# Kernel optimization log

Hardware: AMD Instinct MI355X
Metric: run time of the kernel (lower is better)

Reference implementation:

```python
import jax, jax.numpy as jnp
import numpy as np

DROPOUT_P = 0.0  # undefined global `dropout_p` in source; pinned to 0 (identity) for determinism


def setup_inputs() -> dict:
    key = jax.random.key(0)
    k1, k2, k3 = jax.random.split(key, 3)
    B, Lq, Lk, D = 16, 4096, 4096, 64
    return {
        "query": jax.random.normal(k1, (B, Lq, D), dtype=jnp.float32),
        "key": jax.random.normal(k2, (B, Lk, D), dtype=jnp.float32),
        "value": jax.random.normal(k3, (B, Lk, D), dtype=jnp.float32),
        "scale_factor": jnp.ones((1,), dtype=jnp.float32),
    }


def reference(query, key, value, scale_factor):
    # scores: [B, Lq, Lk] -- the large HBM-materialized intermediate
    scores = jnp.einsum("bqd,bkd->bqk", query, key) / scale_factor
    probs = jax.nn.softmax(scores, axis=-1)
    # dropout with p = DROPOUT_P = 0.0 is the identity
    out = jnp.einsum("bqk,bkd->bqd", probs, value)
    return out
```

## Files before the change

### kernel.cpp

```cpp
#include <hip/hip_runtime.h>
#include <hip/hip_fp16.h>

typedef _Float16 half2_t __attribute__((ext_vector_type(2)));
typedef _Float16 half4_t __attribute__((ext_vector_type(4)));
typedef _Float16 half8_t __attribute__((ext_vector_type(8)));
typedef float   float4_t __attribute__((ext_vector_type(4)));

static __device__ __forceinline__ half2_t cvt_pk(float a, float b) {
    return __builtin_bit_cast(half2_t, __builtin_amdgcn_cvt_pkrtz(a, b));
}
static __device__ __forceinline__ half4_t cvt_pk4(float a, float b, float c, float d) {
    half2_t lo = cvt_pk(a, b), hi = cvt_pk(c, d);
    half4_t r;
    r[0] = lo[0]; r[1] = lo[1]; r[2] = hi[0]; r[3] = hi[1];
    return r;
}
static __device__ __forceinline__ half8_t cvt_pk8(const float4& a, const float4& b) {
    half4_t lo = cvt_pk4(a.x, a.y, a.z, a.w);
    half4_t hi = cvt_pk4(b.x, b.y, b.z, b.w);
    return __builtin_shufflevector(lo, hi, 0, 1, 2, 3, 4, 5, 6, 7);
}

namespace {
constexpr int kB       = 16;
constexpr int kL       = 4096;
constexpr int kD       = 64;
constexpr int kQTile   = 128;
constexpr int kBK      = 64;
constexpr int kTiles   = kL / kBK;
constexpr int kTileH   = kBK * kD;
constexpr int kKStride = 72;
constexpr int kVStride = 68;
constexpr size_t kWsHalves = (size_t)kB * kTiles * kTileH;
}


__global__ __launch_bounds__(256) void prep_kv(const float* __restrict__ K,
                                               const float* __restrict__ V,
                                               _Float16* __restrict__ Kws,
                                               _Float16* __restrict__ Vws)
{
    int blk = blockIdx.x;
    const int tid = threadIdx.x;
    if (blk < kB * kTiles) {
        const float* src = K + (size_t)blk * kTileH;
        _Float16* dst = Kws + (size_t)blk * kTileH;
#pragma unroll
        for (int i = 0; i < 2; ++i) {
            const int task = tid + 256 * i;
            const float* p = src + task * 8;
            const float4 a  = *(const float4*)p;
            const float4 b2 = *(const float4*)(p + 4);
            *(half8_t*)(dst + task * 8) = cvt_pk8(a, b2);
        }
    } else {
        blk -= kB * kTiles;
        const float* src = V + (size_t)blk * kTileH;
        _Float16* dst = Vws + (size_t)blk * kTileH;
        const int d  = tid & 63;
        const int vw = tid >> 6;
#pragma unroll
        for (int i = 0; i < 2; ++i) {
            const int c8 = vw * 2 + i;
            const int k0 = c8 * 8;
            float p[8];
#pragma unroll
            for (int j = 0; j < 8; ++j) p[j] = src[(k0 + j) * kD + d];
            half4_t lo = cvt_pk4(p[0], p[1], p[2], p[3]);
            half4_t hi = cvt_pk4(p[4], p[5], p[6], p[7]);
            *(half8_t*)(dst + (c8 * 64 + d) * 8) =
                __builtin_shufflevector(lo, hi, 0, 1, 2, 3, 4, 5, 6, 7);
        }
    }
}

__global__ __launch_bounds__(256, 2)
void fa_fwd(const float* __restrict__ Q, const _Float16* __restrict__ Kws,
            const _Float16* __restrict__ Vws, const float* __restrict__ scale_ptr,
            float* __restrict__ Out)
{
    __shared__ __align__(16) _Float16 Ksh[kBK * kKStride];
    __shared__ __align__(16) _Float16 Vsh[kD * kVStride];

    const int tid  = threadIdx.x;
    const int wave = tid >> 6;
    const int lane = tid & 63;
    const int c    = lane & 15;
    const int qd   = lane >> 4;

    const int b  = blockIdx.y;
    const int q0 = blockIdx.x * kQTile + wave * 32;

    const int task0 = tid, task1 = tid + 256;
    const int vd = tid & 63;
    const int vw = tid >> 6;

    const float qscale = 1.4426950408889634f / scale_ptr[0];

    const float*    Qb = Q   + (size_t)b * kL * kD;
    const _Float16* Kt = Kws + (size_t)b * kTiles * kTileH;
    const _Float16* Vt = Vws + (size_t)b * kTiles * kTileH;

    half8_t qfrag[2][2];
#pragma unroll
    for (int qt = 0; qt < 2; ++qt) {
        const float* qrow = Qb + (size_t)(q0 + qt * 16 + c) * kD;
#pragma unroll
        for (int dk = 0; dk < 2; ++dk) {
            const float* p = qrow + dk * 32 + qd * 8;
            half8_t h;
#pragma unroll
            for (int j = 0; j < 8; ++j) h[j] = (_Float16)(p[j] * qscale);
            qfrag[qt][dk] = h;
        }
    }

    float4_t O[2][4];
    float4_t O5[2];
#pragma unroll
    for (int qt = 0; qt < 2; ++qt) {
        O5[qt] = (float4_t)0.0f;
#pragma unroll
        for (int dt = 0; dt < 4; ++dt) O[qt][dt] = (float4_t)0.0f;
    }
    float m_run[2] = {-__builtin_inff(), -__builtin_inff()};

    const half4_t vone = {(_Float16)1.0f, (_Float16)1.0f, (_Float16)1.0f, (_Float16)1.0f};

    half8_t kp[2], vp[2];
    kp[0] = *(const half8_t*)(Kt + task0 * 8);
    kp[1] = *(const half8_t*)(Kt + task1 * 8);
    vp[0] = *(const half8_t*)(Vt + ((vw * 2 + 0) * 64 + vd) * 8);
    vp[1] = *(const half8_t*)(Vt + ((vw * 2 + 1) * 64 + vd) * 8);

    for (int t = 0; t < kTiles; ++t) {
        __syncthreads();

        *(half8_t*)(&Ksh[(task0 >> 3) * kKStride + (task0 & 7) * 8]) = kp[0];
        *(half8_t*)(&Ksh[(task1 >> 3) * kKStride + (task1 & 7) * 8]) = kp[1];
#pragma unroll
        for (int i = 0; i < 2; ++i) {
            const int c8 = vw * 2 + i;
            *(half4_t*)(&Vsh[vd * kVStride + c8 * 8])     =
                __builtin_shufflevector(vp[i], vp[i], 0, 1, 2, 3);
            *(half4_t*)(&Vsh[vd * kVStride + c8 * 8 + 4]) =
                __builtin_shufflevector(vp[i], vp[i], 4, 5, 6, 7);
        }
        __syncthreads();

        {
            const int nt = (t + 1) & (kTiles - 1);
            const _Float16* kn = Kt + (size_t)nt * kTileH;
            const _Float16* vn = Vt + (size_t)nt * kTileH;
            kp[0] = *(const half8_t*)(kn + task0 * 8);
            kp[1] = *(const half8_t*)(kn + task1 * 8);
            vp[0] = *(const half8_t*)(vn + ((vw * 2 + 0) * 64 + vd) * 8);
            vp[1] = *(const half8_t*)(vn + ((vw * 2 + 1) * 64 + vd) * 8);
        }

        half8_t kf[4][2];
#pragma unroll
        for (int kt = 0; kt < 4; ++kt)
#pragma unroll
            for (int dk = 0; dk < 2; ++dk)
                kf[kt][dk] = *(const half8_t*)(&Ksh[(kt * 16 + c) * kKStride + dk * 32 + qd * 8]);

        float4_t S[4][2];
#pragma unroll
        for (int kt = 0; kt < 4; ++kt)
#pragma unroll
            for (int qt = 0; qt < 2; ++qt) {
                float4_t acc = {-32.0f, -32.0f, -32.0f, -32.0f};
                acc = __builtin_amdgcn_mfma_f32_16x16x32_f16(kf[kt][0], qfrag[qt][0], acc, 0, 0, 0);
                acc = __builtin_amdgcn_mfma_f32_16x16x32_f16(kf[kt][1], qfrag[qt][1], acc, 0, 0, 0);
                S[kt][qt] = acc;
            }

        half4_t pf[4][2];
#pragma unroll
        for (int qt = 0; qt < 2; ++qt) {
            float tm = S[0][qt][0];
#pragma unroll
            for (int kt = 0; kt < 4; ++kt)
#pragma unroll
                for (int r = 0; r < 4; ++r) tm = fmaxf(tm, S[kt][qt][r]);
            tm = fmaxf(tm, __shfl_xor(tm, 16));
            tm = fmaxf(tm, __shfl_xor(tm, 32));

            const bool newmax = tm > m_run[qt];
            const float mn = newmax ? tm : m_run[qt];
            if (__ballot(newmax)) {
                const float alpha = __builtin_amdgcn_exp2f(m_run[qt] - mn);
                m_run[qt] = mn;
#pragma unroll
                for (int r = 0; r < 4; ++r) {
                    const float a = __shfl(alpha, qd * 4 + r);
#pragma unroll
                    for (int dt = 0; dt < 4; ++dt) O[qt][dt][r] *= a;
                    O5[qt][r] *= a;
                }
            }

#pragma unroll
            for (int kt = 0; kt < 4; ++kt) {
                const float p0 = __builtin_amdgcn_exp2f(S[kt][qt][0] - mn);
                const float p1 = __builtin_amdgcn_exp2f(S[kt][qt][1] - mn);
                const float p2 = __builtin_amdgcn_exp2f(S[kt][qt][2] - mn);
                const float p3 = __builtin_amdgcn_exp2f(S[kt][qt][3] - mn);
                pf[kt][qt] = cvt_pk4(p0, p1, p2, p3);
            }
        }

#pragma unroll
        for (int kt = 0; kt < 4; ++kt) {
#pragma unroll
            for (int dt = 0; dt < 4; ++dt) {
                const half4_t vf = *(const half4_t*)(
                    &Vsh[(dt * 16 + c) * kVStride + kt * 16 + qd * 4]);
#pragma unroll
                for (int qt = 0; qt < 2; ++qt)
                    O[qt][dt] = __builtin_amdgcn_mfma_f32_16x16x16f16(pf[kt][qt], vf, O[qt][dt], 0, 0, 0);
            }
#pragma unroll
            for (int qt = 0; qt < 2; ++qt)
                O5[qt] = __builtin_amdgcn_mfma_f32_16x16x16f16(pf[kt][qt], vone, O5[qt], 0, 0, 0);
        }
    }

#pragma unroll
    for (int qt = 0; qt < 2; ++qt)
#pragma unroll
        for (int r = 0; r < 4; ++r) {
            const float inv = 1.0f / O5[qt][r];
            const int qrow  = q0 + qt * 16 + qd * 4 + r;
            float* op = Out + ((size_t)b * kL + qrow) * kD;
#pragma unroll
            for (int dt = 0; dt < 4; ++dt)
                op[dt * 16 + c] = O[qt][dt][r] * inv;
        }
}

extern "C" void kernel_launch(void* const* d_in, const int* in_sizes, int n_in,
                              void* d_out, int out_size, void* d_ws, size_t ws_size,
                              hipStream_t stream) {
    const float* Q = (const float*)d_in[0];
    const float* K = (const float*)d_in[1];
    const float* V = (const float*)d_in[2];
    const float* s = (const float*)d_in[3];
    float* out = (float*)d_out;
    _Float16* Kws = (_Float16*)d_ws;
    _Float16* Vws = Kws + kWsHalves;

    prep_kv<<<dim3(2 * kB * kTiles), dim3(256), 0, stream>>>(K, V, Kws, Vws);
    fa_fwd<<<dim3(kL / kQTile, kB, 1), dim3(256), 0, stream>>>(Q, Kws, Vws, s, out);
}
```

Baseline: 200.9 us.

## Split KV sequence across two blocks per query tile and merge partials

```diff
diff --git a/kernel.cpp b/kernel.cpp
--- a/kernel.cpp
+++ b/kernel.cpp
@@ -28,10 +28,13 @@
 constexpr int kQTile   = 128;
 constexpr int kBK      = 64;
 constexpr int kTiles   = kL / kBK;
+constexpr int kSplit   = 2;
+constexpr int kTilesHf = kTiles / kSplit;
 constexpr int kTileH   = kBK * kD;
 constexpr int kKStride = 72;
 constexpr int kVStride = 68;
 constexpr size_t kWsHalves = (size_t)kB * kTiles * kTileH;
+constexpr size_t kOHalves  = (size_t)kB * kL * kD;
 }
 
 
@@ -77,7 +80,8 @@
 __global__ __launch_bounds__(256, 2)
 void fa_fwd(const float* __restrict__ Q, const _Float16* __restrict__ Kws,
             const _Float16* __restrict__ Vws, const float* __restrict__ scale_ptr,
-            float* __restrict__ Out)
+            float* __restrict__ Out, _Float16* __restrict__ O2ws,
+            float* __restrict__ Mlws)
 {
     __shared__ __align__(16) _Float16 Ksh[kBK * kKStride];
     __shared__ __align__(16) _Float16 Vsh[kD * kVStride];
@@ -89,6 +93,7 @@
     const int qd   = lane >> 4;
 
     const int b  = blockIdx.y;
+    const int hf = blockIdx.z;
     const int q0 = blockIdx.x * kQTile + wave * 32;
 
     const int task0 = tid, task1 = tid + 256;
@@ -98,8 +103,8 @@
     const float qscale = 1.4426950408889634f / scale_ptr[0];
 
     const float*    Qb = Q   + (size_t)b * kL * kD;
-    const _Float16* Kt = Kws + (size_t)b * kTiles * kTileH;
-    const _Float16* Vt = Vws + (size_t)b * kTiles * kTileH;
+    const _Float16* Kt = Kws + ((size_t)b * kTiles + (size_t)hf * kTilesHf) * kTileH;
+    const _Float16* Vt = Vws + ((size_t)b * kTiles + (size_t)hf * kTilesHf) * kTileH;
 
     half8_t qfrag[2][2];
 #pragma unroll
@@ -133,7 +138,7 @@
     vp[0] = *(const half8_t*)(Vt + ((vw * 2 + 0) * 64 + vd) * 8);
     vp[1] = *(const half8_t*)(Vt + ((vw * 2 + 1) * 64 + vd) * 8);
 
-    for (int t = 0; t < kTiles; ++t) {
+    for (int t = 0; t < kTilesHf; ++t) {
         __syncthreads();
 
         *(half8_t*)(&Ksh[(task0 >> 3) * kKStride + (task0 & 7) * 8]) = kp[0];
@@ -149,7 +154,7 @@
         __syncthreads();
 
         {
-            const int nt = (t + 1) & (kTiles - 1);
+            const int nt = (t + 1) & (kTilesHf - 1);
             const _Float16* kn = Kt + (size_t)nt * kTileH;
             const _Float16* vn = Vt + (size_t)nt * kTileH;
             kp[0] = *(const half8_t*)(kn + task0 * 8);
@@ -231,13 +236,57 @@
     for (int qt = 0; qt < 2; ++qt)
 #pragma unroll
         for (int r = 0; r < 4; ++r) {
-            const float inv = 1.0f / O5[qt][r];
+            const float l   = O5[qt][r];
+            const float inv = 1.0f / l;
+            const float mrow = __shfl(m_run[qt], qd * 4 + r);
             const int qrow  = q0 + qt * 16 + qd * 4 + r;
-            float* op = Out + ((size_t)b * kL + qrow) * kD;
-#pragma unroll
-            for (int dt = 0; dt < 4; ++dt)
-                op[dt * 16 + c] = O[qt][dt][r] * inv;
-        }
+            if (hf == 0) {
+                float* op = Out + ((size_t)b * kL + qrow) * kD;
+#pragma unroll
+                for (int dt = 0; dt < 4; ++dt)
+                    op[dt * 16 + c] = O[qt][dt][r] * inv;
+            } else {
+                _Float16* op = O2ws + ((size_t)b * kL + qrow) * kD;
+#pragma unroll
+                for (int dt = 0; dt < 4; ++dt)
+                    op[dt * 16 + c] = (_Float16)(O[qt][dt][r] * inv);
+            }
+            if (c == 0) {
+                float* mp = Mlws + (((size_t)b * kL + qrow) * 2 + hf) * 2;
+                mp[0] = mrow;
+                mp[1] = l;
+            }
+        }
+}
+
+__global__ __launch_bounds__(256)
+void combine(float* __restrict__ Out, const _Float16* __restrict__ O2ws,
+             const float* __restrict__ Mlws)
+{
+    const int t   = threadIdx.x;
+    const int row = blockIdx.x * 16 + (t >> 4);
+    const int d0  = (t & 15) * 4;
+
+    const float m1 = Mlws[(size_t)row * 4 + 0];
+    const float l1 = Mlws[(size_t)row * 4 + 1];
+    const float m2 = Mlws[(size_t)row * 4 + 2];
+    const float l2 = Mlws[(size_t)row * 4 + 3];
+
+    const float m  = fmaxf(m1, m2);
+    float w1 = l1 * exp2f(m1 - m);
+    float w2 = l2 * exp2f(m2 - m);
+    const float inv = 1.0f / (w1 + w2);
+    w1 *= inv; w2 *= inv;
+
+    float* op = Out + (size_t)row * kD + d0;
+    const _Float16* o2 = O2ws + (size_t)row * kD + d0;
+    float4 a = *(const float4*)op;
+    const half4_t h = *(const half4_t*)o2;
+    a.x = a.x * w1 + (float)h[0] * w2;
+    a.y = a.y * w1 + (float)h[1] * w2;
+    a.z = a.z * w1 + (float)h[2] * w2;
+    a.w = a.w * w1 + (float)h[3] * w2;
+    *(float4*)op = a;
 }
 
 extern "C" void kernel_launch(void* const* d_in, const int* in_sizes, int n_in,
@@ -248,9 +297,12 @@
     const float* V = (const float*)d_in[2];
     const float* s = (const float*)d_in[3];
     float* out = (float*)d_out;
-    _Float16* Kws = (_Float16*)d_ws;
-    _Float16* Vws = Kws + kWsHalves;
+    _Float16* Kws  = (_Float16*)d_ws;
+    _Float16* Vws  = Kws + kWsHalves;
+    _Float16* O2ws = Vws + kWsHalves;
+    float*    Mlws = (float*)(O2ws + kOHalves);
 
     prep_kv<<<dim3(2 * kB * kTiles), dim3(256), 0, stream>>>(K, V, Kws, Vws);
-    fa_fwd<<<dim3(kL / kQTile, kB, 1), dim3(256), 0, stream>>>(Q, Kws, Vws, s, out);
-}
+    fa_fwd<<<dim3(kL / kQTile, kB, kSplit), dim3(256), 0, stream>>>(Q, Kws, Vws, s, out, O2ws, Mlws);
+    combine<<<dim3(kB * kL / 16), dim3(256), 0, stream>>>(out, O2ws, Mlws);
+}
```

Result: no change. 202.0 us (+0.6%).
